# Optimization experiments

Measured on AMD Instinct MI355X. Metric: run time of the kernel, lower is better.

Reference implementation:

```python
import jax, jax.numpy as jnp
import numpy as np

DIM = 256
NUM_HEADS = 8
HEAD_DIM = DIM // NUM_HEADS
WS = 7                 # window_size
N = WS * WS            # tokens per window
B = 4096               # batch * num_windows


def _make_rel_index(ws):
    coords = np.stack(np.meshgrid(np.arange(ws), np.arange(ws), indexing='ij'))  # [2,ws,ws]
    cf = coords.reshape(2, -1)                                                   # [2,N]
    rel = cf[:, :, None] - cf[:, None, :]                                        # [2,N,N]
    rel = rel.transpose(1, 2, 0).copy()
    rel[:, :, 0] += ws - 1
    rel[:, :, 1] += ws - 1
    rel[:, :, 0] *= 2 * ws - 1
    return rel.sum(-1).astype(np.int32)                                          # [N,N]


def setup_inputs() -> dict:
    key = jax.random.key(0)
    ks = jax.random.split(key, 6)
    x = jax.random.normal(ks[0], (B, N, DIM), dtype=jnp.float32)
    qkv_w = jax.random.normal(ks[1], (3 * DIM, DIM), dtype=jnp.float32) * 0.02
    qkv_b = jax.random.normal(ks[2], (3 * DIM,), dtype=jnp.float32) * 0.02
    proj_w = jax.random.normal(ks[3], (DIM, DIM), dtype=jnp.float32) * 0.02
    proj_b = jax.random.normal(ks[4], (DIM,), dtype=jnp.float32) * 0.02
    bias_table = jax.random.normal(ks[5], ((2 * WS - 1) ** 2, NUM_HEADS), dtype=jnp.float32) * 0.02
    rel_index = jnp.asarray(_make_rel_index(WS))
    return {"x": x, "qkv_w": qkv_w, "qkv_b": qkv_b, "proj_w": proj_w,
            "proj_b": proj_b, "bias_table": bias_table, "rel_index": rel_index}


def reference(x, qkv_w, qkv_b, proj_w, proj_b, bias_table, rel_index):
    B_, n, C = x.shape
    scale = HEAD_DIM ** (-0.5)
    # qkv projection -> [3, B, H, N, hd]
    qkv = (x @ qkv_w.T + qkv_b).reshape(B_, n, 3, NUM_HEADS, HEAD_DIM)
    qkv = qkv.transpose(2, 0, 3, 1, 4)
    q, k, v = qkv[0], qkv[1], qkv[2]
    attn = jnp.einsum('bhnd,bhmd->bhnm', q * scale, k)
    # relative position bias gather: [N,N,H] -> [1,H,N,N]
    rel_bias = bias_table[rel_index]                       # [N,N,H]
    attn = attn + rel_bias.transpose(2, 0, 1)[None]
    attn = jax.nn.softmax(attn, axis=-1)
    out = jnp.einsum('bhnm,bhmd->bhnd', attn, v)           # [B,H,N,hd]
    out = out.transpose(0, 2, 1, 3).reshape(B_, n, C)
    return out @ proj_w.T + proj_b
```

## Files before the change

kernel.cpp:

```cpp
#include <hip/hip_runtime.h>
#include <hip/hip_bf16.h>
#include <stdint.h>

#define NWIN 4096

typedef __attribute__((ext_vector_type(8))) short bf16x8;
typedef __attribute__((ext_vector_type(4))) float f32x4;

#define OFF_WQ 0LL
#define OFF_WP 393216LL
#define OFF_RB 524288LL
#define OFF_B  655360LL
#define OFF_Q  1048576LL
#define QKV_STRIDE 102760448LL
#define OFF_K  (OFF_Q + QKV_STRIDE)
#define OFF_V  (OFF_Q + 2 * QKV_STRIDE)

static __device__ __forceinline__ uint32_t f2bf(float f) {
    union { float f; uint32_t u; } v; v.f = f;
    return (v.u + 0x7FFFu + ((v.u >> 16) & 1u)) >> 16;
}

static __device__ __forceinline__ uint32_t pk2(float lo, float hi) {
    union { __hip_bfloat162 h; uint32_t u; } c;
    c.h = __float22bfloat162_rn(float2{lo, hi});
    return c.u;
}

union FragU { uint32_t u[4]; bf16x8 v; };

__global__ void prep_kernel(const float* __restrict__ qkv_w, const float* __restrict__ proj_w,
                            const float* __restrict__ qkv_b,
                            const float* __restrict__ bias_table, const int* __restrict__ rel_index,
                            char* __restrict__ ws) {
    uint16_t* wq  = (uint16_t*)(ws + OFF_WQ);
    uint16_t* wp  = (uint16_t*)(ws + OFF_WP);
    float*    rb  = (float*)(ws + OFF_RB);
    float*    wsb = (float*)(ws + OFF_B);
    const int total = 196608 + 65536 + 32768 + 768;
    for (int idx = blockIdx.x * blockDim.x + threadIdx.x; idx < total;
         idx += gridDim.x * blockDim.x) {
        if (idx < 196608) {
            wq[idx] = (uint16_t)f2bf(qkv_w[idx]);
        } else if (idx < 262144) {
            int i = idx - 196608;
            wp[i] = (uint16_t)f2bf(proj_w[i]);
        } else if (idx < 294912) {
            int i = idx - 262144;
            int h = i >> 12, kt4 = (i >> 8) & 15, qt = (i >> 2) & 63, ii = i & 3;
            int kt = kt4 * 4 + ii;
            float v = -1e30f;
            if (kt < 49 && qt < 49)
                v = bias_table[rel_index[qt * 49 + kt] * 8 + h] * 1.4426950408889634f;
            rb[i] = v;
        } else {
            int n = idx - 294912;
            wsb[n] = qkv_b[n];
        }
    }
}

__global__ __launch_bounds__(256, 2) void qkv_kernel(const float* __restrict__ x,
                                                     char* __restrict__ ws) {
    __shared__ __align__(16) char smem[32768];
    uint16_t* A  = (uint16_t*)smem;
    uint16_t* Bt = (uint16_t*)(smem + 16384);
    const uint16_t* wq  = (const uint16_t*)(ws + OFF_WQ);
    const float*    wsb = (const float*)(ws + OFF_B);
    const int P = blockIdx.x;
    const int s = P / 48, r = P % 48;
    const int g = s * 8 + (r & 7);
    const int m0 = g * 128, n0 = (r >> 3) * 128;
    const int t = threadIdx.x, l = t & 63, w = t >> 6;
    const int lr = l & 15, lg = l >> 4;
    const int wm = w >> 1, wn = w & 1;
    f32x4 acc[4][4];
    #pragma unroll
    for (int a = 0; a < 4; ++a)
        #pragma unroll
        for (int b2 = 0; b2 < 4; ++b2) acc[a][b2] = (f32x4){0.f, 0.f, 0.f, 0.f};

    for (int kk = 0; kk < 4; ++kk) {
        #pragma unroll
        for (int it = 0; it < 4; ++it) {
            int item = it * 256 + t;
            int rr = item >> 3, ch = item & 7;
            const float* src = x + (int64_t)(m0 + rr) * 256 + kk * 64 + ch * 8;
            float4 v0 = *(const float4*)src;
            float4 v1 = *(const float4*)(src + 4);
            uint4 pk;
            pk.x = pk2(v0.x, v0.y); pk.y = pk2(v0.z, v0.w);
            pk.z = pk2(v1.x, v1.y); pk.w = pk2(v1.z, v1.w);
            *(uint4*)((char*)A + ((rr * 128 + ch * 16) ^ ((rr & 7) << 4))) = pk;
        }
        #pragma unroll
        for (int it = 0; it < 4; ++it) {
            int item = it * 256 + t;
            int rr = item >> 3, ch = item & 7;
            uint4 v = *(const uint4*)(wq + (int64_t)(n0 + rr) * 256 + kk * 64 + ch * 8);
            *(uint4*)((char*)Bt + ((rr * 128 + ch * 16) ^ ((rr & 7) << 4))) = v;
        }
        __syncthreads();
        #pragma unroll
        for (int kh = 0; kh < 2; ++kh) {
            bf16x8 af[4], bfr[4];
            #pragma unroll
            for (int mi = 0; mi < 4; ++mi) {
                int rr = wm * 64 + 16 * mi + lr;
                af[mi] = *(const bf16x8*)((char*)A + ((rr * 128 + kh * 64 + lg * 16) ^ ((rr & 7) << 4)));
            }
            #pragma unroll
            for (int nj = 0; nj < 4; ++nj) {
                int rr = wn * 64 + 16 * nj + lr;
                bfr[nj] = *(const bf16x8*)((char*)Bt + ((rr * 128 + kh * 64 + lg * 16) ^ ((rr & 7) << 4)));
            }
            #pragma unroll
            for (int nj = 0; nj < 4; ++nj)
                #pragma unroll
                for (int mi = 0; mi < 4; ++mi)
                    acc[nj][mi] = __builtin_amdgcn_mfma_f32_16x16x32_bf16(bfr[nj], af[mi], acc[nj][mi], 0, 0, 0);
        }
        __syncthreads();
    }
    uint16_t* C = (uint16_t*)smem;
    #pragma unroll
    for (int nj = 0; nj < 4; ++nj) {
        f32x4 bias = *(const f32x4*)(wsb + n0 + wn * 64 + 16 * nj + 4 * lg);
        #pragma unroll
        for (int mi = 0; mi < 4; ++mi) {
            int tok_l = wm * 64 + 16 * mi + lr;
            int nb = wn * 64 + 16 * nj + 4 * lg;
            uint2 pk;
            pk.x = pk2(acc[nj][mi][0] + bias[0], acc[nj][mi][1] + bias[1]);
            pk.y = pk2(acc[nj][mi][2] + bias[2], acc[nj][mi][3] + bias[3]);
            *(uint2*)((char*)C + ((tok_l * 256 + nb * 2) ^ ((tok_l & 7) << 4))) = pk;
        }
    }
    __syncthreads();
    const int sel = n0 >> 8;
    char* dstBase = ws + OFF_Q + (int64_t)sel * QKV_STRIDE;
    #pragma unroll
    for (int it = 0; it < 8; ++it) {
        int hh = it >> 1;
        int mrow = ((it & 1) << 6) | (t >> 2);
        int q4 = t & 3;
        uint4 v = *(const uint4*)((char*)C + ((mrow * 256 + hh * 64 + q4 * 16) ^ ((mrow & 7) << 4)));
        int m = m0 + mrow;
        int b = m / 49;
        int tok = m - b * 49;
        int h = ((n0 >> 5) + hh) & 7;
        *(uint4*)(dstBase + (((int64_t)b * 8 + h) * 49 + tok) * 64 + q4 * 16) = v;
    }
}

__global__ __launch_bounds__(512, 2) void attn_kernel(char* __restrict__ ws) {
    __shared__ __align__(16) char smem[32768];
    const int b = blockIdx.x;
    const int t = threadIdx.x, l = t & 63, w = t >> 6;
    const int lr = l & 15, lg = l >> 4;
    const uint16_t* Q = (const uint16_t*)(ws + OFF_Q);
    const uint16_t* K = (const uint16_t*)(ws + OFF_K);
    const uint16_t* V = (const uint16_t*)(ws + OFF_V);
    const float*   rb = (const float*)(ws + OFF_RB);
    char* VL = smem + w * 4096;
    char* OL = smem;
    const float scale = 0.17677669529663687f * 1.4426950408889634f;
    const int64_t bh = (int64_t)b * 8 + w;

    uint4 vstage[4];
    int   vc[4];
    #pragma unroll
    for (int it = 0; it < 4; ++it) {
        int item = it * 64 + l;
        int tok = item >> 2, d0 = (item & 3) * 8;
        int a = tok >> 4, g = (tok >> 2) & 3, ii = tok & 3;
        vc[it] = (a >> 1) * 32 + g * 8 + (a & 1) * 4 + ii;
        uint4 v = {0u, 0u, 0u, 0u};
        if (tok < 49) v = *(const uint4*)(V + (bh * 49 + tok) * 32 + d0);
        vstage[it] = v;
    }

    bf16x8 qf[4], kf[4];
    #pragma unroll
    for (int nj = 0; nj < 4; ++nj)
        qf[nj] = *(const bf16x8*)(Q + (bh * 49 + 16 * nj + lr) * 32 + lg * 8);
    #pragma unroll
    for (int mj = 0; mj < 4; ++mj)
        kf[mj] = *(const bf16x8*)(K + (bh * 49 + 16 * mj + lr) * 32 + lg * 8);

    float rs[4];
    bf16x8 pf[4][2];
    #pragma unroll
    for (int nj = 0; nj < 4; ++nj) {
        f32x4 s[4];
        __builtin_amdgcn_s_setprio(1);
        #pragma unroll
        for (int mj = 0; mj < 4; ++mj)
            s[mj] = __builtin_amdgcn_mfma_f32_16x16x32_bf16(
                kf[mj], qf[nj], (f32x4){0.f, 0.f, 0.f, 0.f}, 0, 0, 0);
        __builtin_amdgcn_s_setprio(0);
        #pragma unroll
        for (int mj = 0; mj < 4; ++mj) {
            f32x4 rbv = *(const f32x4*)(rb + ((w * 16 + 4 * mj + lg) * 64 + 16 * nj + lr) * 4);
            s[mj] = s[mj] * scale + rbv;
        }
        float m = s[0][0];
        #pragma unroll
        for (int mj = 0; mj < 4; ++mj)
            #pragma unroll
            for (int i = 0; i < 4; ++i) m = fmaxf(m, s[mj][i]);
        m = fmaxf(m, __shfl_xor(m, 16));
        m = fmaxf(m, __shfl_xor(m, 32));
        float sum = 0.f;
        #pragma unroll
        for (int mj = 0; mj < 4; ++mj)
            #pragma unroll
            for (int i = 0; i < 4; ++i) {
                float e = __builtin_amdgcn_exp2f(s[mj][i] - m);
                s[mj][i] = e;
                sum += e;
            }
        sum += __shfl_xor(sum, 16);
        sum += __shfl_xor(sum, 32);
        rs[nj] = sum;
        #pragma unroll
        for (int ks = 0; ks < 2; ++ks) {
            FragU f;
            f.u[0] = pk2(s[2 * ks][0], s[2 * ks][1]);
            f.u[1] = pk2(s[2 * ks][2], s[2 * ks][3]);
            f.u[2] = pk2(s[2 * ks + 1][0], s[2 * ks + 1][1]);
            f.u[3] = pk2(s[2 * ks + 1][2], s[2 * ks + 1][3]);
            pf[nj][ks] = f.v;
        }
    }

    #pragma unroll
    for (int it = 0; it < 4; ++it) {
        int item = it * 64 + l;
        int d0 = (item & 3) * 8;
        int c = vc[it];
        const uint32_t words[4] = {vstage[it].x, vstage[it].y, vstage[it].z, vstage[it].w};
        #pragma unroll
        for (int jj = 0; jj < 4; ++jj) {
            int dA = d0 + 2 * jj, dB = dA + 1;
            *(uint16_t*)(VL + ((dA * 128 + c * 2) ^ ((dA & 7) << 4))) = (uint16_t)words[jj];
            *(uint16_t*)(VL + ((dB * 128 + c * 2) ^ ((dB & 7) << 4))) = (uint16_t)(words[jj] >> 16);
        }
    }
    bf16x8 vf[2][2];
    #pragma unroll
    for (int dt = 0; dt < 2; ++dt)
        #pragma unroll
        for (int ks = 0; ks < 2; ++ks) {
            int row = dt * 16 + lr;
            vf[dt][ks] = *(const bf16x8*)(VL + ((row * 128 + ks * 64 + lg * 16) ^ ((row & 7) << 4)));
        }

    f32x4 o[2][4];
    __builtin_amdgcn_s_setprio(1);
    #pragma unroll
    for (int dt = 0; dt < 2; ++dt)
        #pragma unroll
        for (int nj = 0; nj < 4; ++nj) {
            f32x4 acc = __builtin_amdgcn_mfma_f32_16x16x32_bf16(
                vf[dt][0], pf[nj][0], (f32x4){0.f, 0.f, 0.f, 0.f}, 0, 0, 0);
            o[dt][nj] = __builtin_amdgcn_mfma_f32_16x16x32_bf16(vf[dt][1], pf[nj][1], acc, 0, 0, 0);
        }
    __builtin_amdgcn_s_setprio(0);

    __syncthreads();
    #pragma unroll
    for (int nj = 0; nj < 4; ++nj) {
        const float rinv = 1.0f / rs[nj];
        const int row = 16 * nj + lr;
        const int swz = (row & 7) << 4;
        #pragma unroll
        for (int dt = 0; dt < 2; ++dt) {
            uint2 pk;
            pk.x = pk2(o[dt][nj][0] * rinv, o[dt][nj][1] * rinv);
            pk.y = pk2(o[dt][nj][2] * rinv, o[dt][nj][3] * rinv);
            *(uint2*)(OL + ((row * 512 + w * 64 + dt * 32 + lg * 8) ^ swz)) = pk;
        }
    }
    __syncthreads();
    char* OWS = ws + OFF_V;
    #pragma unroll
    for (int it = 0; it < 4; ++it) {
        int c = it * 512 + t;
        if (c < 1568) {
            int tok = c >> 5, ch = c & 31;
            uint4 v = *(const uint4*)(OL + ((tok * 512 + ch * 16) ^ ((tok & 7) << 4)));
            *(uint4*)(OWS + ((int64_t)b * 49 + tok) * 512 + ch * 16) = v;
        }
    }
}

__global__ __launch_bounds__(256, 2) void proj_kernel(const float* __restrict__ proj_b,
                                                      float* __restrict__ out,
                                                      const char* __restrict__ ws) {
    __shared__ __align__(16) char smem[65536];
    uint16_t* A  = (uint16_t*)smem;
    uint16_t* Bt = (uint16_t*)(smem + 16384);
    const uint16_t* OWS = (const uint16_t*)(ws + OFF_V);
    const uint16_t* wp  = (const uint16_t*)(ws + OFF_WP);
    const int P = blockIdx.x;
    const int s = P / 16, r = P % 16;
    const int g = s * 8 + (r & 7);
    const int m0 = g * 128, n0 = (r >> 3) * 128;
    const int t = threadIdx.x, l = t & 63, w = t >> 6;
    const int lr = l & 15, lg = l >> 4;
    const int wm = w >> 1, wn = w & 1;
    f32x4 acc[4][4];
    #pragma unroll
    for (int a = 0; a < 4; ++a)
        #pragma unroll
        for (int b2 = 0; b2 < 4; ++b2) acc[a][b2] = (f32x4){0.f, 0.f, 0.f, 0.f};

    for (int kk = 0; kk < 4; ++kk) {
        #pragma unroll
        for (int it = 0; it < 4; ++it) {
            int item = it * 256 + t;
            int rr = item >> 3, ch = item & 7;
            uint4 va = *(const uint4*)(OWS + (int64_t)(m0 + rr) * 256 + kk * 64 + ch * 8);
            *(uint4*)((char*)A + ((rr * 128 + ch * 16) ^ ((rr & 7) << 4))) = va;
            uint4 vb = *(const uint4*)(wp + (int64_t)(n0 + rr) * 256 + kk * 64 + ch * 8);
            *(uint4*)((char*)Bt + ((rr * 128 + ch * 16) ^ ((rr & 7) << 4))) = vb;
        }
        __syncthreads();
        #pragma unroll
        for (int kh = 0; kh < 2; ++kh) {
            bf16x8 af[4], bfr[4];
            #pragma unroll
            for (int mi = 0; mi < 4; ++mi) {
                int rr = wm * 64 + 16 * mi + lr;
                af[mi] = *(const bf16x8*)((char*)A + ((rr * 128 + kh * 64 + lg * 16) ^ ((rr & 7) << 4)));
            }
            #pragma unroll
            for (int nj = 0; nj < 4; ++nj) {
                int rr = wn * 64 + 16 * nj + lr;
                bfr[nj] = *(const bf16x8*)((char*)Bt + ((rr * 128 + kh * 64 + lg * 16) ^ ((rr & 7) << 4)));
            }
            #pragma unroll
            for (int nj = 0; nj < 4; ++nj)
                #pragma unroll
                for (int mi = 0; mi < 4; ++mi)
                    acc[nj][mi] = __builtin_amdgcn_mfma_f32_16x16x32_bf16(bfr[nj], af[mi], acc[nj][mi], 0, 0, 0);
        }
        __syncthreads();
    }
    float* C = (float*)smem;
    #pragma unroll
    for (int nj = 0; nj < 4; ++nj)
        #pragma unroll
        for (int mi = 0; mi < 4; ++mi) {
            int tok_l = wm * 64 + 16 * mi + lr;
            int nb = wn * 64 + 16 * nj + 4 * lg;
            *(f32x4*)((char*)C + ((tok_l * 512 + nb * 4) ^ ((tok_l & 7) << 4))) = acc[nj][mi];
        }
    __syncthreads();
    #pragma unroll
    for (int it = 0; it < 16; ++it) {
        int c = it * 256 + t;
        int mrow = c >> 5, ch = c & 31;
        f32x4 v = *(const f32x4*)((char*)C + ((mrow * 512 + ch * 16) ^ ((mrow & 7) << 4)));
        f32x4 bias = *(const f32x4*)(proj_b + n0 + ch * 4);
        v = v + bias;
        *(f32x4*)(out + (int64_t)(m0 + mrow) * 256 + n0 + ch * 4) = v;
    }
}

extern "C" void kernel_launch(void* const* d_in, const int* in_sizes, int n_in,
                              void* d_out, int out_size, void* d_ws, size_t ws_size,
                              hipStream_t stream) {
    const float* x          = (const float*)d_in[0];
    const float* qkv_w      = (const float*)d_in[1];
    const float* qkv_b      = (const float*)d_in[2];
    const float* proj_w     = (const float*)d_in[3];
    const float* proj_b     = (const float*)d_in[4];
    const float* bias_table = (const float*)d_in[5];
    const int*   rel_index  = (const int*)d_in[6];
    float* out = (float*)d_out;
    char*  ws  = (char*)d_ws;

    prep_kernel<<<1155, 256, 0, stream>>>(qkv_w, proj_w, qkv_b, bias_table, rel_index, ws);
    qkv_kernel<<<9408, 256, 0, stream>>>(x, ws);
    attn_kernel<<<NWIN, 512, 0, stream>>>(ws);
    proj_kernel<<<3136, 256, 0, stream>>>(proj_b, out, ws);
}
```

Measured before the change: 327.7 us.

## Fuse output projection into attention kernel and drop separate proj kernel

The attention kernel now multiplies the per-window attention output held in LDS directly by the projection weights using MFMA, adds the bias and writes fp32 results to the output. This removes the bf16 intermediate write and re-read through global memory and one kernel launch. In exchange each window block loads the full projection weight matrix from global or L2 without LDS tiling, and the final stores are scattered scalar writes with padded rows (64 computed for 49 tokens).

```diff
diff --git a/kernel.cpp b/kernel.cpp
--- a/kernel.cpp
+++ b/kernel.cpp
@@ -153,7 +153,9 @@
     }
 }
 
-__global__ __launch_bounds__(512, 2) void attn_kernel(char* __restrict__ ws) {
+__global__ __launch_bounds__(512, 2) void attn_kernel(const float* __restrict__ proj_b,
+                                                      float* __restrict__ out,
+                                                      const char* __restrict__ ws) {
     __shared__ __align__(16) char smem[32768];
     const int b = blockIdx.x;
     const int t = threadIdx.x, l = t & 63, w = t >> 6;
@@ -161,6 +163,7 @@
     const uint16_t* Q = (const uint16_t*)(ws + OFF_Q);
     const uint16_t* K = (const uint16_t*)(ws + OFF_K);
     const uint16_t* V = (const uint16_t*)(ws + OFF_V);
+    const uint16_t* wp = (const uint16_t*)(ws + OFF_WP);
     const float*   rb = (const float*)(ws + OFF_RB);
     char* VL = smem + w * 4096;
     char* OL = smem;
@@ -283,89 +286,41 @@
         }
     }
     __syncthreads();
-    char* OWS = ws + OFF_V;
-    #pragma unroll
-    for (int it = 0; it < 4; ++it) {
-        int c = it * 512 + t;
-        if (c < 1568) {
-            int tok = c >> 5, ch = c & 31;
-            uint4 v = *(const uint4*)(OL + ((tok * 512 + ch * 16) ^ ((tok & 7) << 4)));
-            *(uint4*)(OWS + ((int64_t)b * 49 + tok) * 512 + ch * 16) = v;
-        }
-    }
-}
-
-__global__ __launch_bounds__(256, 2) void proj_kernel(const float* __restrict__ proj_b,
-                                                      float* __restrict__ out,
-                                                      const char* __restrict__ ws) {
-    __shared__ __align__(16) char smem[65536];
-    uint16_t* A  = (uint16_t*)smem;
-    uint16_t* Bt = (uint16_t*)(smem + 16384);
-    const uint16_t* OWS = (const uint16_t*)(ws + OFF_V);
-    const uint16_t* wp  = (const uint16_t*)(ws + OFF_WP);
-    const int P = blockIdx.x;
-    const int s = P / 16, r = P % 16;
-    const int g = s * 8 + (r & 7);
-    const int m0 = g * 128, n0 = (r >> 3) * 128;
-    const int t = threadIdx.x, l = t & 63, w = t >> 6;
-    const int lr = l & 15, lg = l >> 4;
-    const int wm = w >> 1, wn = w & 1;
-    f32x4 acc[4][4];
-    #pragma unroll
-    for (int a = 0; a < 4; ++a)
-        #pragma unroll
-        for (int b2 = 0; b2 < 4; ++b2) acc[a][b2] = (f32x4){0.f, 0.f, 0.f, 0.f};
-
-    for (int kk = 0; kk < 4; ++kk) {
-        #pragma unroll
-        for (int it = 0; it < 4; ++it) {
-            int item = it * 256 + t;
-            int rr = item >> 3, ch = item & 7;
-            uint4 va = *(const uint4*)(OWS + (int64_t)(m0 + rr) * 256 + kk * 64 + ch * 8);
-            *(uint4*)((char*)A + ((rr * 128 + ch * 16) ^ ((rr & 7) << 4))) = va;
-            uint4 vb = *(const uint4*)(wp + (int64_t)(n0 + rr) * 256 + kk * 64 + ch * 8);
-            *(uint4*)((char*)Bt + ((rr * 128 + ch * 16) ^ ((rr & 7) << 4))) = vb;
-        }
-        __syncthreads();
-        #pragma unroll
-        for (int kh = 0; kh < 2; ++kh) {
-            bf16x8 af[4], bfr[4];
-            #pragma unroll
-            for (int mi = 0; mi < 4; ++mi) {
-                int rr = wm * 64 + 16 * mi + lr;
-                af[mi] = *(const bf16x8*)((char*)A + ((rr * 128 + kh * 64 + lg * 16) ^ ((rr & 7) << 4)));
+
+    f32x4 pacc[4][2];
+    #pragma unroll
+    for (int mi = 0; mi < 4; ++mi)
+        #pragma unroll
+        for (int nj = 0; nj < 2; ++nj)
+            pacc[mi][nj] = (f32x4){0.f, 0.f, 0.f, 0.f};
+    #pragma unroll
+    for (int kk = 0; kk < 8; ++kk) {
+        bf16x8 av[4];
+        #pragma unroll
+        for (int mi = 0; mi < 4; ++mi) {
+            const int row = mi * 16 + lr;
+            av[mi] = *(const bf16x8*)(OL + ((row * 512 + kk * 64 + lg * 16) ^ ((row & 7) << 4)));
+        }
+        #pragma unroll
+        for (int nj = 0; nj < 2; ++nj) {
+            bf16x8 bv = *(const bf16x8*)(wp + (w * 32 + nj * 16 + lr) * 256 + kk * 32 + lg * 8);
+            #pragma unroll
+            for (int mi = 0; mi < 4; ++mi)
+                pacc[mi][nj] = __builtin_amdgcn_mfma_f32_16x16x32_bf16(av[mi], bv, pacc[mi][nj], 0, 0, 0);
+        }
+    }
+    #pragma unroll
+    for (int nj = 0; nj < 2; ++nj) {
+        const int n = w * 32 + nj * 16 + lr;
+        const float pb = proj_b[n];
+        #pragma unroll
+        for (int mi = 0; mi < 4; ++mi)
+            #pragma unroll
+            for (int i = 0; i < 4; ++i) {
+                const int tok = mi * 16 + lg * 4 + i;
+                if (tok < 49)
+                    out[((int64_t)b * 49 + tok) * 256 + n] = pacc[mi][nj][i] + pb;
             }
-            #pragma unroll
-            for (int nj = 0; nj < 4; ++nj) {
-                int rr = wn * 64 + 16 * nj + lr;
-                bfr[nj] = *(const bf16x8*)((char*)Bt + ((rr * 128 + kh * 64 + lg * 16) ^ ((rr & 7) << 4)));
-            }
-            #pragma unroll
-            for (int nj = 0; nj < 4; ++nj)
-                #pragma unroll
-                for (int mi = 0; mi < 4; ++mi)
-                    acc[nj][mi] = __builtin_amdgcn_mfma_f32_16x16x32_bf16(bfr[nj], af[mi], acc[nj][mi], 0, 0, 0);
-        }
-        __syncthreads();
-    }
-    float* C = (float*)smem;
-    #pragma unroll
-    for (int nj = 0; nj < 4; ++nj)
-        #pragma unroll
-        for (int mi = 0; mi < 4; ++mi) {
-            int tok_l = wm * 64 + 16 * mi + lr;
-            int nb = wn * 64 + 16 * nj + 4 * lg;
-            *(f32x4*)((char*)C + ((tok_l * 512 + nb * 4) ^ ((tok_l & 7) << 4))) = acc[nj][mi];
-        }
-    __syncthreads();
-    #pragma unroll
-    for (int it = 0; it < 16; ++it) {
-        int c = it * 256 + t;
-        int mrow = c >> 5, ch = c & 31;
-        f32x4 v = *(const f32x4*)((char*)C + ((mrow * 512 + ch * 16) ^ ((mrow & 7) << 4)));
-        f32x4 bias = *(const f32x4*)(proj_b + n0 + ch * 4);
-        v = v + bias;
-        *(f32x4*)(out + (int64_t)(m0 + mrow) * 256 + n0 + ch * 4) = v;
     }
 }
 
@@ -384,6 +339,5 @@
 
     prep_kernel<<<1155, 256, 0, stream>>>(qkv_w, proj_w, qkv_b, bias_table, rel_index, ws);
     qkv_kernel<<<9408, 256, 0, stream>>>(x, ws);
-    attn_kernel<<<NWIN, 512, 0, stream>>>(ws);
-    proj_kernel<<<3136, 256, 0, stream>>>(proj_b, out, ws);
-}
+    attn_kernel<<<NWIN, 512, 0, stream>>>(proj_b, out, ws);
+}
```

Result: faster. 315.5 us, median of 2 (-3.7%).
